# Kernel optimization log

Hardware: AMD Instinct MI355X
Metric: run time of the kernel (lower is better)

## Reference

```python
import jax, jax.numpy as jnp
import numpy as np

N_NODES = 50000
N_EDGES = 800000
IN_CH = 128
HID = 64
PROJ = 32


def _gcn_norm(edge_index, n):
    # add self loops, symmetric normalization D^-1/2 (A+I) D^-1/2
    loop = jnp.arange(n, dtype=edge_index.dtype)
    src = jnp.concatenate([edge_index[0], loop])
    dst = jnp.concatenate([edge_index[1], loop])
    deg = jax.ops.segment_sum(jnp.ones_like(dst, jnp.float32), dst, num_segments=n)
    dinv = deg ** -0.5  # deg >= 1 due to self loops
    norm = dinv[src] * dinv[dst]
    return src, dst, norm


def _propagate(h, src, dst, norm, n):
    # gather -> scale -> scatter-add (message passing along A_hat)
    return jax.ops.segment_sum(h[src] * norm[:, None], dst, num_segments=n)


def _ho_gcn_layer(x, src, dst, norm, Ws, b, n):
    # out = sum_{k=1..max_order} (A_hat^k x) W_k + b
    out = jnp.zeros((n, Ws[0].shape[1]), x.dtype)
    h = x
    for W in Ws:
        h = _propagate(h, src, dst, norm, n)
        out = out + h @ W
    return out + b


def setup_inputs() -> dict:
    key = jax.random.key(0)
    ks = jax.random.split(key, 16)

    def w(k, fan_in, fan_out):
        return (jax.random.normal(k, (fan_in, fan_out), jnp.float32) / np.sqrt(fan_in)).astype(jnp.float32)

    x = jax.random.normal(ks[0], (N_NODES, IN_CH), jnp.float32)
    edge_index = jax.random.randint(ks[1], (2, N_EDGES), 0, N_NODES, dtype=jnp.int64)
    return {
        "x": x,
        "edge_index": edge_index,
        # conv1: max_order=2 -> two weights
        "W1_1": w(ks[2], IN_CH, HID), "W1_2": w(ks[3], IN_CH, HID),
        "b1": jnp.zeros((HID,), jnp.float32),
        # conv2
        "W2_1": w(ks[4], HID, HID // 2), "W2_2": w(ks[5], HID, HID // 2),
        "b2": jnp.zeros((HID // 2,), jnp.float32),
        # projection head
        "Wp1": w(ks[6], HID // 2, PROJ), "bp1": jnp.zeros((PROJ,), jnp.float32),
        "Wp2": w(ks[7], PROJ, PROJ), "bp2": jnp.zeros((PROJ,), jnp.float32),
        # coordinate head
        "Wc1": w(ks[8], HID // 2, HID // 4), "bc1": jnp.zeros((HID // 4,), jnp.float32),
        "Wc2": w(ks[9], HID // 4, 2), "bc2": jnp.zeros((2,), jnp.float32),
    }


def reference(x, edge_index, W1_1, W1_2, b1, W2_1, W2_2, b2,
              Wp1, bp1, Wp2, bp2, Wc1, bc1, Wc2, bc2):
    n = x.shape[0]
    src, dst, norm = _gcn_norm(edge_index, n)
    h1 = jax.nn.relu(_ho_gcn_layer(x, src, dst, norm, (W1_1, W1_2), b1, n))
    # dropout is identity in eval/reference mode
    h2 = jax.nn.relu(_ho_gcn_layer(h1, src, dst, norm, (W2_1, W2_2), b2, n))
    z = jax.nn.relu(h2 @ Wp1 + bp1) @ Wp2 + bp2
    coordinates = jax.nn.relu(h2 @ Wc1 + bc1) @ Wc2 + bc2
    return (coordinates, z)
```

## Files before the change

kernel.cpp:

```cpp
#include <hip/hip_runtime.h>

#define NN 50000
#define NE 800000
#define S 4
#define BINW 12500
#define NN4 (NN * S)
#define NBLK2 ((NN4 + 255) / 256)
#define NBG ((NN + 63) / 64)
#define NBH4 ((NE / 4 + 255) / 256)
#define COLCAP (NE + 3 * NN4 + 8)

__global__ __launch_bounds__(256) void zero_cnt_k(int* __restrict__ cnt,
                                                  float* __restrict__ y1s,
                                                  float* __restrict__ y2s,
                                                  float* __restrict__ z1s,
                                                  float* __restrict__ z2s) {
    int i = blockIdx.x * blockDim.x + threadIdx.x;
    if (i < NN4) cnt[i] = 0;
    if (blockIdx.x == 0) {
        int t = threadIdx.x;
        if (t < 64) { y1s[t] = 0.f; y2s[t] = 0.f; }
        else if (t < 96) { z1s[t - 64] = 0.f; z2s[t - 64] = 0.f; }
    }
}

__global__ __launch_bounds__(256) void hist_k(const int* __restrict__ src,
                                              const int* __restrict__ dst,
                                              int* __restrict__ cnt,
                                              int* __restrict__ rank) {
    int e = (blockIdx.x * 256 + threadIdx.x) * 4;
    if (e >= NE) return;
    int4 s4 = *(const int4*)(src + e);
    int4 d4 = *(const int4*)(dst + e);
    int4 r;
    r.x = atomicAdd(&cnt[d4.x * S + s4.x / BINW], 1);
    r.y = atomicAdd(&cnt[d4.y * S + s4.y / BINW], 1);
    r.z = atomicAdd(&cnt[d4.z * S + s4.z / BINW], 1);
    r.w = atomicAdd(&cnt[d4.w * S + s4.w / BINW], 1);
    *(int4*)(rank + e) = r;
}

__global__ __launch_bounds__(256) void sum_blocks_k(const int* __restrict__ cnt,
                                                    int* __restrict__ bsum,
                                                    float* __restrict__ dinv) {
    __shared__ int s[256];
    int t = threadIdx.x;
    int i = blockIdx.x * 256 + t;
    int v = 0;
    if (i < NN4) {
        int c = cnt[i];
        v = (c + 3) & ~3;
        if ((i & 3) == 0) {
            int deg = c + cnt[i + 1] + cnt[i + 2] + cnt[i + 3];
            dinv[i >> 2] = rsqrtf((float)(deg + 1));
        }
    }
    s[t] = v;
    __syncthreads();
    for (int off = 128; off > 0; off >>= 1) {
        if (t < off) s[t] += s[t + off];
        __syncthreads();
    }
    if (t == 0) bsum[blockIdx.x] = s[0];
}

__global__ __launch_bounds__(256) void scan_final_k(const int* __restrict__ cnt,
                                                    const int* __restrict__ bsum,
                                                    int* __restrict__ rowsS) {
    __shared__ int sOff[256];
    __shared__ int s[256];
    int t = threadIdx.x;
    int accum = 0;
    for (int idx = t; idx < NBLK2; idx += 256)
        if (idx < blockIdx.x) accum += bsum[idx];
    sOff[t] = accum;
    __syncthreads();
    for (int off = 128; off > 0; off >>= 1) {
        if (t < off) sOff[t] += sOff[t + off];
        __syncthreads();
    }
    int boff = sOff[0];

    int i = blockIdx.x * 256 + t;
    int v = (i < NN4) ? ((cnt[i] + 3) & ~3) : 0;
    s[t] = v;
    __syncthreads();
    for (int off = 1; off < 256; off <<= 1) {
        int x = (t >= off) ? s[t - off] : 0;
        __syncthreads();
        s[t] += x;
        __syncthreads();
    }
    if (i < NN4) rowsS[i] = boff + s[t] - v;
    if (blockIdx.x == NBLK2 - 1 && t == 255) rowsS[NN4] = boff + s[t];
}

__global__ __launch_bounds__(256) void gemm1_scatter_k(const float* __restrict__ A,
                                                       const float* __restrict__ WA,
                                                       const float* __restrict__ WB,
                                                       float* __restrict__ outA,
                                                       float* __restrict__ outB,
                                                       const int* __restrict__ src,
                                                       const int* __restrict__ dst,
                                                       const int* __restrict__ rank,
                                                       const int* __restrict__ rowsS,
                                                       const int* __restrict__ cnt,
                                                       int* __restrict__ col,
                                                       const float* __restrict__ dinv) {
    if (blockIdx.x >= NBG) {
        int idx = (blockIdx.x - NBG) * 256 + threadIdx.x;
        int e = idx * 4;
        if (e < NE) {
            int4 s4 = *(const int4*)(src + e);
            int4 d4 = *(const int4*)(dst + e);
            int4 r4 = *(const int4*)(rank + e);
            col[rowsS[d4.x * S + s4.x / BINW] + r4.x] = s4.x;
            col[rowsS[d4.y * S + s4.y / BINW] + r4.y] = s4.y;
            col[rowsS[d4.z * S + s4.z / BINW] + r4.z] = s4.z;
            col[rowsS[d4.w * S + s4.w / BINW] + r4.w] = s4.w;
        }
        if (idx < NN4) {
            int end = rowsS[idx] + cnt[idx];
            int nxt = rowsS[idx + 1];
            for (int i = end; i < nxt; i++) col[i] = NN;
        }
        return;
    }

    __shared__ float As[64 * 36];
    __shared__ float W1s[32 * 68];
    __shared__ float W2s[32 * 68];
    const int t = threadIdx.x;
    const int tj = t & 15;
    const int tn = t >> 4;
    const int n0 = blockIdx.x * 64;
    float acc[4][8] = {};

    for (int kc = 0; kc < 128; kc += 32) {
        if (kc) __syncthreads();
        {
            int idx = t;
#pragma unroll
            for (int r = 0; r < 2; r++, idx += 256) {
                int nl = idx >> 3, q = idx & 7;
                int node = n0 + nl; node = node < NN ? node : NN - 1;
                float4 a = ((const float4*)A)[(size_t)node * 32 + (kc >> 2) + q];
                *(float4*)&As[nl * 36 + q * 4] = a;
            }
        }
        {
            int idx = t;
#pragma unroll
            for (int r = 0; r < 2; r++, idx += 256) {
                int kl = idx >> 4, j4 = idx & 15;
                *(float4*)&W1s[kl * 68 + j4 * 4] = ((const float4*)WA)[(size_t)(kc + kl) * 16 + j4];
                *(float4*)&W2s[kl * 68 + j4 * 4] = ((const float4*)WB)[(size_t)(kc + kl) * 16 + j4];
            }
        }
        __syncthreads();

        const float* ap = &As[tn * 4 * 36];
        const float* w1p = &W1s[tj * 4];
        const float* w2p = &W2s[tj * 4];
#pragma unroll 2
        for (int k4 = 0; k4 < 8; k4++) {
            float4 a0 = *(const float4*)&ap[0 * 36 + k4 * 4];
            float4 a1 = *(const float4*)&ap[1 * 36 + k4 * 4];
            float4 a2 = *(const float4*)&ap[2 * 36 + k4 * 4];
            float4 a3 = *(const float4*)&ap[3 * 36 + k4 * 4];
#pragma unroll
            for (int kk = 0; kk < 4; kk++) {
                float4 w1 = *(const float4*)&w1p[(k4 * 4 + kk) * 68];
                float4 w2 = *(const float4*)&w2p[(k4 * 4 + kk) * 68];
                float av0 = kk == 0 ? a0.x : kk == 1 ? a0.y : kk == 2 ? a0.z : a0.w;
                float av1 = kk == 0 ? a1.x : kk == 1 ? a1.y : kk == 2 ? a1.z : a1.w;
                float av2 = kk == 0 ? a2.x : kk == 1 ? a2.y : kk == 2 ? a2.z : a2.w;
                float av3 = kk == 0 ? a3.x : kk == 1 ? a3.y : kk == 2 ? a3.z : a3.w;
#define FMA8(m, AV)                                                     \
                acc[m][0] += AV * w1.x; acc[m][1] += AV * w1.y;          \
                acc[m][2] += AV * w1.z; acc[m][3] += AV * w1.w;          \
                acc[m][4] += AV * w2.x; acc[m][5] += AV * w2.y;          \
                acc[m][6] += AV * w2.z; acc[m][7] += AV * w2.w;
                FMA8(0, av0)
                FMA8(1, av1)
                FMA8(2, av2)
                FMA8(3, av3)
#undef FMA8
            }
        }
    }

#pragma unroll
    for (int m = 0; m < 4; m++) {
        int node = n0 + tn * 4 + m;
        if (node < NN) {
            float dnm = dinv[node];
            *(float4*)&outA[(size_t)node * 64 + tj * 4] =
                make_float4(acc[m][0], acc[m][1], acc[m][2], acc[m][3]);
            *(float4*)&outB[(size_t)node * 64 + tj * 4] =
                make_float4(dnm * acc[m][4], dnm * acc[m][5],
                            dnm * acc[m][6], dnm * acc[m][7]);
        }
    }
}

template<int LOG2C4, bool ADDIN>
__global__ __launch_bounds__(256) void prop_k(const float4* __restrict__ h4,
                                              const float4* __restrict__ addin4,
                                              const float* __restrict__ bias,
                                              float4* __restrict__ out4,
                                              const int* __restrict__ rowsS,
                                              const int* __restrict__ col,
                                              const float* __restrict__ dinv) {
    const int C4 = 1 << LOG2C4;
    unsigned tid = blockIdx.x * blockDim.x + threadIdx.x;
    unsigned node = tid >> LOG2C4;
    if (node >= NN) return;
    unsigned lane = tid & (C4 - 1);
    size_t rowoff = ((size_t)node << LOG2C4) + lane;
    float dn = dinv[node];
    float4 g = h4[rowoff];
    int rs = rowsS[node * S];
    int re = rowsS[node * S + S];
    int4 c = *(const int4*)(col + rs);
    for (int i = rs; i < re; i += 4) {
        int4 cc = c;
        c = *(const int4*)(col + i + 4);
        float4 v0 = h4[((size_t)cc.x << LOG2C4) + lane];
        float4 v1 = h4[((size_t)cc.y << LOG2C4) + lane];
        float4 v2 = h4[((size_t)cc.z << LOG2C4) + lane];
        float4 v3 = h4[((size_t)cc.w << LOG2C4) + lane];
        g.x += v0.x + v1.x + v2.x + v3.x;
        g.y += v0.y + v1.y + v2.y + v3.y;
        g.z += v0.z + v1.z + v2.z + v3.z;
        g.w += v0.w + v1.w + v2.w + v3.w;
    }
    float4 acc;
    if (ADDIN) {
        float4 a = addin4[rowoff];
        acc.x = dn * (a.x + dn * g.x);
        acc.y = dn * (a.y + dn * g.y);
        acc.z = dn * (a.z + dn * g.z);
        acc.w = dn * (a.w + dn * g.w);
    } else {
        float4 b = ((const float4*)bias)[lane];
        acc.x = fmaxf(b.x + dn * g.x, 0.0f);
        acc.y = fmaxf(b.y + dn * g.y, 0.0f);
        acc.z = fmaxf(b.z + dn * g.z, 0.0f);
        acc.w = fmaxf(b.w + dn * g.w, 0.0f);
    }
    out4[rowoff] = acc;
}

template<int K, int JW>
__global__ __launch_bounds__(256) void gemm_k(const float* __restrict__ A,
                                              const float* __restrict__ WA,
                                              const float* __restrict__ WB,
                                              float* __restrict__ outA,
                                              float* __restrict__ outB, int n,
                                              const float* __restrict__ dinv) {
    __shared__ float As[64 * 68];
    __shared__ float Ws[64 * 68];
    const int t = threadIdx.x;
    const int tj = t & 15;
    const int tn = t >> 4;
    const int n0 = blockIdx.x * 64;
    float acc[4][4] = {};

    for (int kc = 0; kc < K; kc += 64) {
        if (kc) __syncthreads();
        {
            int idx = t;
#pragma unroll
            for (int r = 0; r < 4; r++, idx += 256) {
                int nl = idx >> 4, q = idx & 15;
                int node = n0 + nl; node = node < n ? node : n - 1;
                float4 a = ((const float4*)A)[(size_t)node * (K / 4) + (kc >> 2) + q];
                *(float4*)&As[nl * 68 + q * 4] = a;
            }
        }
        {
            int idx = t;
#pragma unroll
            for (int r = 0; r < 4; r++, idx += 256) {
                int kl = idx >> 4, j4 = idx & 15;
                const float* W = (j4 < 8) ? WA : WB;
                float4 w = ((const float4*)W)[(size_t)(kc + kl) * 8 + (j4 & 7)];
                *(float4*)&Ws[kl * 68 + j4 * 4] = w;
            }
        }
        __syncthreads();

        const float* ap = &As[tn * 4 * 68];
        const float* wp = &Ws[tj * 4];
#pragma unroll 4
        for (int k4 = 0; k4 < 16; k4++) {
            float4 a0 = *(const float4*)&ap[0 * 68 + k4 * 4];
            float4 a1 = *(const float4*)&ap[1 * 68 + k4 * 4];
            float4 a2 = *(const float4*)&ap[2 * 68 + k4 * 4];
            float4 a3 = *(const float4*)&ap[3 * 68 + k4 * 4];
            float4 w0 = *(const float4*)&wp[(k4 * 4 + 0) * 68];
            float4 w1 = *(const float4*)&wp[(k4 * 4 + 1) * 68];
            float4 w2 = *(const float4*)&wp[(k4 * 4 + 2) * 68];
            float4 w3 = *(const float4*)&wp[(k4 * 4 + 3) * 68];
#define FMA_ROW(m, AV)                                                   \
            acc[m][0] += AV.x * w0.x + AV.y * w1.x + AV.z * w2.x + AV.w * w3.x; \
            acc[m][1] += AV.x * w0.y + AV.y * w1.y + AV.z * w2.y + AV.w * w3.y; \
            acc[m][2] += AV.x * w0.z + AV.y * w1.z + AV.z * w2.z + AV.w * w3.z; \
            acc[m][3] += AV.x * w0.w + AV.y * w1.w + AV.z * w2.w + AV.w * w3.w;
            FMA_ROW(0, a0)
            FMA_ROW(1, a1)
            FMA_ROW(2, a2)
            FMA_ROW(3, a3)
#undef FMA_ROW
        }
    }

    int mat = tj >> 3;
    float* ob = (mat ? outB : outA) + (tj & 7) * 4;
#pragma unroll
    for (int m = 0; m < 4; m++) {
        int node = n0 + tn * 4 + m;
        if (node < n) {
            float sc = mat ? dinv[node] : 1.0f;
            *(float4*)&ob[(size_t)node * JW] =
                make_float4(sc * acc[m][0], sc * acc[m][1],
                            sc * acc[m][2], sc * acc[m][3]);
        }
    }
}

__global__ __launch_bounds__(256) void prop_heads_k(const float4* __restrict__ h4,
                                                    const float* __restrict__ b2,
                                                    const int* __restrict__ rowsS,
                                                    const int* __restrict__ col,
                                                    const float* __restrict__ dinv,
                                                    const float* __restrict__ Wp1, const float* __restrict__ bp1,
                                                    const float* __restrict__ Wp2, const float* __restrict__ bp2,
                                                    const float* __restrict__ Wc1, const float* __restrict__ bc1,
                                                    const float* __restrict__ Wc2, const float* __restrict__ bc2,
                                                    float* __restrict__ coord, float* __restrict__ z) {
    __shared__ float sWp1[32 * 32], sWp2[32 * 32], sWc1[32 * 16], sWc2[32];
    __shared__ float sbp1[32], sbp2[32], sbc1[16], sbc2[2];
    __shared__ float sh[32 * 36], st[32 * 36], stc[32 * 18];
    const int t = threadIdx.x;
    for (int i = t; i < 1024; i += 256) { sWp1[i] = Wp1[i]; sWp2[i] = Wp2[i]; }
    for (int i = t; i < 512; i += 256) sWc1[i] = Wc1[i];
    if (t < 32) { sWc2[t] = Wc2[t]; sbp1[t] = bp1[t]; sbp2[t] = bp2[t]; }
    if (t < 16) sbc1[t] = bc1[t];
    if (t < 2) sbc2[t] = bc2[t];

    const int n0 = blockIdx.x * 32;
    const int nl = t >> 3;
    const int jq = t & 7;
    const int node = n0 + nl;

    float4 acc = make_float4(0.f, 0.f, 0.f, 0.f);
    if (node < NN) {
        size_t rowoff = ((size_t)node << 3) + jq;
        float dn = dinv[node];
        float4 g = h4[rowoff];
        int rs = rowsS[node * S];
        int re = rowsS[node * S + S];
        int4 c = *(const int4*)(col + rs);
        for (int i = rs; i < re; i += 4) {
            int4 cc = c;
            c = *(const int4*)(col + i + 4);
            float4 v0 = h4[((size_t)cc.x << 3) + jq];
            float4 v1 = h4[((size_t)cc.y << 3) + jq];
            float4 v2 = h4[((size_t)cc.z << 3) + jq];
            float4 v3 = h4[((size_t)cc.w << 3) + jq];
            g.x += v0.x + v1.x + v2.x + v3.x;
            g.y += v0.y + v1.y + v2.y + v3.y;
            g.z += v0.z + v1.z + v2.z + v3.z;
            g.w += v0.w + v1.w + v2.w + v3.w;
        }
        float4 b = ((const float4*)b2)[jq];
        acc.x = fmaxf(b.x + dn * g.x, 0.0f);
        acc.y = fmaxf(b.y + dn * g.y, 0.0f);
        acc.z = fmaxf(b.z + dn * g.z, 0.0f);
        acc.w = fmaxf(b.w + dn * g.w, 0.0f);
    }
    *(float4*)&sh[nl * 36 + jq * 4] = acc;
    __syncthreads();

    float4 a = *(const float4*)&sbp1[jq * 4];
#pragma unroll
    for (int k = 0; k < 32; k++) {
        float hv = sh[nl * 36 + k];
        float4 w = *(const float4*)&sWp1[k * 32 + jq * 4];
        a.x += hv * w.x; a.y += hv * w.y; a.z += hv * w.z; a.w += hv * w.w;
    }
    a.x = fmaxf(a.x, 0.f); a.y = fmaxf(a.y, 0.f);
    a.z = fmaxf(a.z, 0.f); a.w = fmaxf(a.w, 0.f);
    *(float4*)&st[nl * 36 + jq * 4] = a;

    float2 cc2 = *(const float2*)&sbc1[jq * 2];
#pragma unroll
    for (int k = 0; k < 32; k++) {
        float hv = sh[nl * 36 + k];
        float2 w = *(const float2*)&sWc1[k * 16 + jq * 2];
        cc2.x += hv * w.x; cc2.y += hv * w.y;
    }
    cc2.x = fmaxf(cc2.x, 0.f); cc2.y = fmaxf(cc2.y, 0.f);
    *(float2*)&stc[nl * 18 + jq * 2] = cc2;
    __syncthreads();

    float4 zz = *(const float4*)&sbp2[jq * 4];
#pragma unroll
    for (int k = 0; k < 32; k++) {
        float tv = st[nl * 36 + k];
        float4 w = *(const float4*)&sWp2[k * 32 + jq * 4];
        zz.x += tv * w.x; zz.y += tv * w.y; zz.z += tv * w.z; zz.w += tv * w.w;
    }
    if (node < NN) *(float4*)&z[(size_t)node * 32 + jq * 4] = zz;

    if (jq < 2) {
        float s = sbc2[jq];
#pragma unroll
        for (int k = 0; k < 16; k++) s += stc[nl * 18 + k] * sWc2[k * 2 + jq];
        if (node < NN) coord[(size_t)node * 2 + jq] = s;
    }
}

extern "C" void kernel_launch(void* const* d_in, const int* in_sizes, int n_in,
                              void* d_out, int out_size, void* d_ws, size_t ws_size,
                              hipStream_t stream) {
    const float* x    = (const float*)d_in[0];
    const int*   ei   = (const int*)d_in[1];
    const int*   src  = ei;
    const int*   dst  = ei + NE;
    const float* W1_1 = (const float*)d_in[2];
    const float* W1_2 = (const float*)d_in[3];
    const float* b1   = (const float*)d_in[4];
    const float* W2_1 = (const float*)d_in[5];
    const float* W2_2 = (const float*)d_in[6];
    const float* b2   = (const float*)d_in[7];
    const float* Wp1  = (const float*)d_in[8];
    const float* bp1  = (const float*)d_in[9];
    const float* Wp2  = (const float*)d_in[10];
    const float* bp2  = (const float*)d_in[11];
    const float* Wc1  = (const float*)d_in[12];
    const float* bc1  = (const float*)d_in[13];
    const float* Wc2  = (const float*)d_in[14];
    const float* bc2  = (const float*)d_in[15];

    float* ws    = (float*)d_ws;
    float* dinv  = ws;
    int*   cnt   = (int*)(ws + 50004);
    int*   rowsS = cnt + NN4;
    int*   bsum  = rowsS + NN4 + 4;
    int*   rank  = bsum + 1024;
    int*   col   = rank + NE;
    float* bufY  = (float*)(col + COLCAP);
    float* bufZ  = bufY + (size_t)(NN + 1) * 128;

    float* y1 = bufY;
    float* y2 = bufY + (size_t)(NN + 1) * 64;
    float* u  = y1;
    float* h1 = y2;
    float* z1 = bufZ;
    float* z2 = bufZ + (size_t)(NN + 1) * 32;
    float* u2 = z1;

    float* coord = (float*)d_out;
    float* z     = (float*)d_out + 2 * NN;

    zero_cnt_k<<<NBLK2, 256, 0, stream>>>(cnt,
                                          y1 + (size_t)NN * 64, y2 + (size_t)NN * 64,
                                          z1 + (size_t)NN * 32, z2 + (size_t)NN * 32);
    hist_k<<<NBH4, 256, 0, stream>>>(src, dst, cnt, rank);
    sum_blocks_k<<<NBLK2, 256, 0, stream>>>(cnt, bsum, dinv);
    scan_final_k<<<NBLK2, 256, 0, stream>>>(cnt, bsum, rowsS);
    gemm1_scatter_k<<<NBG + NBH4, 256, 0, stream>>>(x, W1_1, W1_2, y1, y2,
                                                    src, dst, rank, rowsS, cnt, col, dinv);

    prop_k<4, true><<<(NN * 16 + 255) / 256, 256, 0, stream>>>(
        (const float4*)y2, (const float4*)y1, nullptr, (float4*)u, rowsS, col, dinv);
    prop_k<4, false><<<(NN * 16 + 255) / 256, 256, 0, stream>>>(
        (const float4*)u, nullptr, b1, (float4*)h1, rowsS, col, dinv);
    gemm_k<64, 32><<<(NN + 63) / 64, 256, 0, stream>>>(h1, W2_1, W2_2, z1, z2, NN, dinv);
    prop_k<3, true><<<(NN * 8 + 255) / 256, 256, 0, stream>>>(
        (const float4*)z2, (const float4*)z1, nullptr, (float4*)u2, rowsS, col, dinv);
    prop_heads_k<<<(NN + 31) / 32, 256, 0, stream>>>(
        (const float4*)u2, b2, rowsS, col, dinv,
        Wp1, bp1, Wp2, bp2, Wc1, bc1, Wc2, bc2, coord, z);
}
```

Baseline: 277.7 us.

## Store gathered propagation features in fp16 to halve gather traffic

```diff
diff --git a/kernel.cpp b/kernel.cpp
--- a/kernel.cpp
+++ b/kernel.cpp
@@ -1,4 +1,5 @@
 #include <hip/hip_runtime.h>
+#include <hip/hip_fp16.h>
 
 #define NN 50000
 #define NE 800000
@@ -10,18 +11,20 @@
 #define NBH4 ((NE / 4 + 255) / 256)
 #define COLCAP (NE + 3 * NN4 + 8)
 
-__global__ __launch_bounds__(256) void zero_cnt_k(int* __restrict__ cnt,
-                                                  float* __restrict__ y1s,
-                                                  float* __restrict__ y2s,
-                                                  float* __restrict__ z1s,
-                                                  float* __restrict__ z2s) {
-    int i = blockIdx.x * blockDim.x + threadIdx.x;
-    if (i < NN4) cnt[i] = 0;
-    if (blockIdx.x == 0) {
-        int t = threadIdx.x;
-        if (t < 64) { y1s[t] = 0.f; y2s[t] = 0.f; }
-        else if (t < 96) { z1s[t - 64] = 0.f; z2s[t - 64] = 0.f; }
-    }
+__device__ __forceinline__ float4 ldh4(const __half2* p) {
+    float2 raw = *(const float2*)p;
+    __half2 a = *(__half2*)&raw.x;
+    __half2 b = *(__half2*)&raw.y;
+    float2 fa = __half22float2(a);
+    float2 fb = __half22float2(b);
+    return make_float4(fa.x, fa.y, fb.x, fb.y);
+}
+__device__ __forceinline__ void sth4(__half2* p, float4 v) {
+    __half2 a = __floats2half2_rn(v.x, v.y);
+    __half2 b = __floats2half2_rn(v.z, v.w);
+    float2 raw;
+    raw.x = *(float*)&a; raw.y = *(float*)&b;
+    *(float2*)p = raw;
 }
 
 __global__ __launch_bounds__(256) void hist_k(const int* __restrict__ src,
@@ -42,10 +45,18 @@
 
 __global__ __launch_bounds__(256) void sum_blocks_k(const int* __restrict__ cnt,
                                                     int* __restrict__ bsum,
-                                                    float* __restrict__ dinv) {
+                                                    float* __restrict__ dinv,
+                                                    unsigned* __restrict__ y2h_s,
+                                                    unsigned* __restrict__ uh_s,
+                                                    unsigned* __restrict__ z2h_s,
+                                                    unsigned* __restrict__ u2h_s) {
     __shared__ int s[256];
     int t = threadIdx.x;
     int i = blockIdx.x * 256 + t;
+    if (blockIdx.x == 0) {
+        if (t < 32) { y2h_s[t] = 0u; uh_s[t] = 0u; }
+        else if (t < 48) { z2h_s[t - 32] = 0u; u2h_s[t - 32] = 0u; }
+    }
     int v = 0;
     if (i < NN4) {
         int c = cnt[i];
@@ -99,7 +110,7 @@
                                                        const float* __restrict__ WA,
                                                        const float* __restrict__ WB,
                                                        float* __restrict__ outA,
-                                                       float* __restrict__ outB,
+                                                       __half2* __restrict__ outBh,
                                                        const int* __restrict__ src,
                                                        const int* __restrict__ dst,
                                                        const int* __restrict__ rank,
@@ -197,39 +208,41 @@
             float dnm = dinv[node];
             *(float4*)&outA[(size_t)node * 64 + tj * 4] =
                 make_float4(acc[m][0], acc[m][1], acc[m][2], acc[m][3]);
-            *(float4*)&outB[(size_t)node * 64 + tj * 4] =
-                make_float4(dnm * acc[m][4], dnm * acc[m][5],
-                            dnm * acc[m][6], dnm * acc[m][7]);
-        }
-    }
-}
-
-template<int LOG2C4, bool ADDIN>
-__global__ __launch_bounds__(256) void prop_k(const float4* __restrict__ h4,
+            sth4(outBh + (size_t)node * 32 + tj * 2,
+                 make_float4(dnm * acc[m][4], dnm * acc[m][5],
+                             dnm * acc[m][6], dnm * acc[m][7]));
+        }
+    }
+}
+
+template<int LOG2C4, bool ADDIN, bool OUTH>
+__global__ __launch_bounds__(256) void prop_k(const __half2* __restrict__ hsrc,
                                               const float4* __restrict__ addin4,
                                               const float* __restrict__ bias,
-                                              float4* __restrict__ out4,
+                                              float4* __restrict__ outf,
+                                              __half2* __restrict__ outh,
                                               const int* __restrict__ rowsS,
                                               const int* __restrict__ col,
                                               const float* __restrict__ dinv) {
     const int C4 = 1 << LOG2C4;
+    const int R2 = 2 * C4;
     unsigned tid = blockIdx.x * blockDim.x + threadIdx.x;
     unsigned node = tid >> LOG2C4;
     if (node >= NN) return;
     unsigned lane = tid & (C4 - 1);
-    size_t rowoff = ((size_t)node << LOG2C4) + lane;
+    size_t lane2 = (size_t)lane * 2;
     float dn = dinv[node];
-    float4 g = h4[rowoff];
-    int rs = rowsS[node * S];
-    int re = rowsS[node * S + S];
+    float4 g = ldh4(hsrc + (size_t)node * R2 + lane2);
+    int rs = rowsS[node << 2];
+    int re = rowsS[(node << 2) + 4];
     int4 c = *(const int4*)(col + rs);
     for (int i = rs; i < re; i += 4) {
         int4 cc = c;
         c = *(const int4*)(col + i + 4);
-        float4 v0 = h4[((size_t)cc.x << LOG2C4) + lane];
-        float4 v1 = h4[((size_t)cc.y << LOG2C4) + lane];
-        float4 v2 = h4[((size_t)cc.z << LOG2C4) + lane];
-        float4 v3 = h4[((size_t)cc.w << LOG2C4) + lane];
+        float4 v0 = ldh4(hsrc + (size_t)cc.x * R2 + lane2);
+        float4 v1 = ldh4(hsrc + (size_t)cc.y * R2 + lane2);
+        float4 v2 = ldh4(hsrc + (size_t)cc.z * R2 + lane2);
+        float4 v3 = ldh4(hsrc + (size_t)cc.w * R2 + lane2);
         g.x += v0.x + v1.x + v2.x + v3.x;
         g.y += v0.y + v1.y + v2.y + v3.y;
         g.z += v0.z + v1.z + v2.z + v3.z;
@@ -237,7 +250,7 @@
     }
     float4 acc;
     if (ADDIN) {
-        float4 a = addin4[rowoff];
+        float4 a = addin4[((size_t)node << LOG2C4) + lane];
         acc.x = dn * (a.x + dn * g.x);
         acc.y = dn * (a.y + dn * g.y);
         acc.z = dn * (a.z + dn * g.z);
@@ -249,7 +262,8 @@
         acc.z = fmaxf(b.z + dn * g.z, 0.0f);
         acc.w = fmaxf(b.w + dn * g.w, 0.0f);
     }
-    out4[rowoff] = acc;
+    if (OUTH) sth4(outh + (size_t)node * R2 + lane2, acc);
+    else      outf[((size_t)node << LOG2C4) + lane] = acc;
 }
 
 template<int K, int JW>
@@ -257,7 +271,7 @@
                                               const float* __restrict__ WA,
                                               const float* __restrict__ WB,
                                               float* __restrict__ outA,
-                                              float* __restrict__ outB, int n,
+                                              __half2* __restrict__ outBh, int n,
                                               const float* __restrict__ dinv) {
     __shared__ float As[64 * 68];
     __shared__ float Ws[64 * 68];
@@ -317,20 +331,25 @@
     }
 
     int mat = tj >> 3;
-    float* ob = (mat ? outB : outA) + (tj & 7) * 4;
+    int jw = tj & 7;
 #pragma unroll
     for (int m = 0; m < 4; m++) {
         int node = n0 + tn * 4 + m;
         if (node < n) {
-            float sc = mat ? dinv[node] : 1.0f;
-            *(float4*)&ob[(size_t)node * JW] =
-                make_float4(sc * acc[m][0], sc * acc[m][1],
-                            sc * acc[m][2], sc * acc[m][3]);
-        }
-    }
-}
-
-__global__ __launch_bounds__(256) void prop_heads_k(const float4* __restrict__ h4,
+            if (mat) {
+                float sc = dinv[node];
+                sth4(outBh + (size_t)node * 16 + jw * 2,
+                     make_float4(sc * acc[m][0], sc * acc[m][1],
+                                 sc * acc[m][2], sc * acc[m][3]));
+            } else {
+                *(float4*)&outA[(size_t)node * JW + jw * 4] =
+                    make_float4(acc[m][0], acc[m][1], acc[m][2], acc[m][3]);
+            }
+        }
+    }
+}
+
+__global__ __launch_bounds__(256) void prop_heads_k(const __half2* __restrict__ hsrc,
                                                     const float* __restrict__ b2,
                                                     const int* __restrict__ rowsS,
                                                     const int* __restrict__ col,
@@ -357,19 +376,19 @@
 
     float4 acc = make_float4(0.f, 0.f, 0.f, 0.f);
     if (node < NN) {
-        size_t rowoff = ((size_t)node << 3) + jq;
+        size_t lane2 = (size_t)jq * 2;
         float dn = dinv[node];
-        float4 g = h4[rowoff];
-        int rs = rowsS[node * S];
-        int re = rowsS[node * S + S];
+        float4 g = ldh4(hsrc + (size_t)node * 16 + lane2);
+        int rs = rowsS[node << 2];
+        int re = rowsS[(node << 2) + 4];
         int4 c = *(const int4*)(col + rs);
         for (int i = rs; i < re; i += 4) {
             int4 cc = c;
             c = *(const int4*)(col + i + 4);
-            float4 v0 = h4[((size_t)cc.x << 3) + jq];
-            float4 v1 = h4[((size_t)cc.y << 3) + jq];
-            float4 v2 = h4[((size_t)cc.z << 3) + jq];
-            float4 v3 = h4[((size_t)cc.w << 3) + jq];
+            float4 v0 = ldh4(hsrc + (size_t)cc.x * 16 + lane2);
+            float4 v1 = ldh4(hsrc + (size_t)cc.y * 16 + lane2);
+            float4 v2 = ldh4(hsrc + (size_t)cc.z * 16 + lane2);
+            float4 v3 = ldh4(hsrc + (size_t)cc.w * 16 + lane2);
             g.x += v0.x + v1.x + v2.x + v3.x;
             g.y += v0.y + v1.y + v2.y + v3.y;
             g.z += v0.z + v1.z + v2.z + v3.z;
@@ -445,44 +464,43 @@
     const float* Wc2  = (const float*)d_in[14];
     const float* bc2  = (const float*)d_in[15];
 
-    float* ws    = (float*)d_ws;
-    float* dinv  = ws;
-    int*   cnt   = (int*)(ws + 50004);
-    int*   rowsS = cnt + NN4;
-    int*   bsum  = rowsS + NN4 + 4;
-    int*   rank  = bsum + 1024;
-    int*   col   = rank + NE;
-    float* bufY  = (float*)(col + COLCAP);
-    float* bufZ  = bufY + (size_t)(NN + 1) * 128;
-
-    float* y1 = bufY;
-    float* y2 = bufY + (size_t)(NN + 1) * 64;
-    float* u  = y1;
-    float* h1 = y2;
-    float* z1 = bufZ;
-    float* z2 = bufZ + (size_t)(NN + 1) * 32;
-    float* u2 = z1;
+    float*   ws    = (float*)d_ws;
+    float*   dinv  = ws;
+    int*     cnt   = (int*)(ws + 50004);
+    int*     rowsS = cnt + NN4;
+    int*     bsum  = rowsS + NN4 + 4;
+    int*     rank  = bsum + 1024;
+    int*     col   = rank + NE;
+    float*   y1    = (float*)(col + COLCAP);
+    float*   z1    = y1 + (size_t)NN * 64;
+    __half2* y2h   = (__half2*)(z1 + (size_t)NN * 32);
+    __half2* uh    = y2h + (size_t)(NN + 1) * 32;
+    __half2* z2h   = uh + (size_t)(NN + 1) * 32;
+    __half2* u2h   = z2h + (size_t)(NN + 1) * 16;
+    float*   h1    = y1;
 
     float* coord = (float*)d_out;
     float* z     = (float*)d_out + 2 * NN;
 
-    zero_cnt_k<<<NBLK2, 256, 0, stream>>>(cnt,
-                                          y1 + (size_t)NN * 64, y2 + (size_t)NN * 64,
-                                          z1 + (size_t)NN * 32, z2 + (size_t)NN * 32);
+    hipMemsetAsync(cnt, 0, NN4 * sizeof(int), stream);
     hist_k<<<NBH4, 256, 0, stream>>>(src, dst, cnt, rank);
-    sum_blocks_k<<<NBLK2, 256, 0, stream>>>(cnt, bsum, dinv);
+    sum_blocks_k<<<NBLK2, 256, 0, stream>>>(cnt, bsum, dinv,
+                                            (unsigned*)(y2h + (size_t)NN * 32),
+                                            (unsigned*)(uh + (size_t)NN * 32),
+                                            (unsigned*)(z2h + (size_t)NN * 16),
+                                            (unsigned*)(u2h + (size_t)NN * 16));
     scan_final_k<<<NBLK2, 256, 0, stream>>>(cnt, bsum, rowsS);
-    gemm1_scatter_k<<<NBG + NBH4, 256, 0, stream>>>(x, W1_1, W1_2, y1, y2,
+    gemm1_scatter_k<<<NBG + NBH4, 256, 0, stream>>>(x, W1_1, W1_2, y1, y2h,
                                                     src, dst, rank, rowsS, cnt, col, dinv);
 
-    prop_k<4, true><<<(NN * 16 + 255) / 256, 256, 0, stream>>>(
-        (const float4*)y2, (const float4*)y1, nullptr, (float4*)u, rowsS, col, dinv);
-    prop_k<4, false><<<(NN * 16 + 255) / 256, 256, 0, stream>>>(
-        (const float4*)u, nullptr, b1, (float4*)h1, rowsS, col, dinv);
-    gemm_k<64, 32><<<(NN + 63) / 64, 256, 0, stream>>>(h1, W2_1, W2_2, z1, z2, NN, dinv);
-    prop_k<3, true><<<(NN * 8 + 255) / 256, 256, 0, stream>>>(
-        (const float4*)z2, (const float4*)z1, nullptr, (float4*)u2, rowsS, col, dinv);
+    prop_k<4, true, true><<<(NN * 16 + 255) / 256, 256, 0, stream>>>(
+        y2h, (const float4*)y1, nullptr, nullptr, uh, rowsS, col, dinv);
+    prop_k<4, false, false><<<(NN * 16 + 255) / 256, 256, 0, stream>>>(
+        uh, nullptr, b1, (float4*)h1, nullptr, rowsS, col, dinv);
+    gemm_k<64, 32><<<(NN + 63) / 64, 256, 0, stream>>>(h1, W2_1, W2_2, z1, z2h, NN, dinv);
+    prop_k<3, true, true><<<(NN * 8 + 255) / 256, 256, 0, stream>>>(
+        z2h, (const float4*)z1, nullptr, nullptr, u2h, rowsS, col, dinv);
     prop_heads_k<<<(NN + 31) / 32, 256, 0, stream>>>(
-        (const float4*)u2, b2, rowsS, col, dinv,
+        u2h, b2, rowsS, col, dinv,
         Wp1, bp1, Wp2, bp2, Wc1, bc1, Wc2, bc2, coord, z);
 }
```

Result: faster. 257.0 us (-7.5%).
